# Kernel optimization log

Hardware: AMD Instinct MI355X
Metric: run time of the kernel (lower is better)

## Reference

```python
import jax, jax.numpy as jnp
import numpy as np
from functools import partial

EPS = 1e-6

def rmsnorm(x, w):
    rms = jnp.sqrt(jnp.mean(x * x, axis=-1, keepdims=True) + EPS)
    return x * w / rms

def causal_dwconv(x, w):
    # x: [B, T, D], w: [D, 1, k] depthwise kernel (torch Conv1d layout)
    D = x.shape[-1]
    k = w.shape[-1]
    xt = jnp.transpose(x, (0, 2, 1))  # [B, D, T]
    out = jax.lax.conv_general_dilated(
        xt, w, window_strides=(1,), padding=[(k - 1, 0)],
        dimension_numbers=("NCH", "OIH", "NCH"), feature_group_count=D)
    return jnp.transpose(out, (0, 2, 1))  # [B, T, D]

def setup_inputs() -> dict:
    key = jax.random.key(0)
    B, T, D, F, S = 2, 4096, 1024, 4096, 4096
    ks = jax.random.split(key, 20)
    s = 0.02
    return {
        "x": jax.random.normal(ks[0], (B, T, D), jnp.float32),
        "h_prev": jnp.zeros((B, D), jnp.float32),
        "norm1_w": jnp.ones((D,), jnp.float32),
        "conv3_w": jax.random.normal(ks[1], (D, 1, 3), jnp.float32) * s,
        "conv7_w": jax.random.normal(ks[2], (D, 1, 7), jnp.float32) * s,
        "conv15_w": jax.random.normal(ks[3], (D, 1, 15), jnp.float32) * s,
        "mix_w": jax.random.normal(ks[4], (D, D), jnp.float32) * s,
        "norm2_w": jnp.ones((D,), jnp.float32),
        "Wz_w": jax.random.normal(ks[5], (D, D), jnp.float32) * s,
        "Wz_b": jnp.zeros((D,), jnp.float32),
        "Wh_w": jax.random.normal(ks[6], (D, D), jnp.float32) * s,
        "Wh_b": jnp.zeros((D,), jnp.float32),
        "norm3_w": jnp.ones((D,), jnp.float32),
        "slot_keys": jax.random.normal(ks[7], (S, D), jnp.float32) * s,
        "slot_values": jax.random.normal(ks[8], (S, D), jnp.float32) * s,
        "projq_w": jax.random.normal(ks[9], (D, D), jnp.float32) * s,
        "projout_w": jax.random.normal(ks[10], (D, D), jnp.float32) * s,
        "norm4_w": jnp.ones((D,), jnp.float32),
        "gate_w": jax.random.normal(ks[11], (F, D), jnp.float32) * s,
        "up_w": jax.random.normal(ks[12], (F, D), jnp.float32) * s,
        "down_w": jax.random.normal(ks[13], (D, F), jnp.float32) * s,
    }

def resonance_forward(x, h_prev, norm1_w, conv3_w, conv7_w, conv15_w, mix_w,
                      norm2_w, Wz_w, Wz_b, Wh_w, Wh_b, norm3_w, slot_keys,
                      slot_values, projq_w, projout_w, norm4_w, gate_w, up_w, down_w):
    B, T, D = x.shape
    top_k = 2
    # 1. multi-scale causal conv block
    xn = rmsnorm(x, norm1_w)
    conv = causal_dwconv(xn, conv3_w) + causal_dwconv(xn, conv7_w) + causal_dwconv(xn, conv15_w)
    x = x + conv @ mix_w.T
    # 2. MinGRU: precompute gates, then linear recurrence via scan
    xn = rmsnorm(x, norm2_w)
    z = jax.nn.sigmoid(xn @ Wz_w.T + Wz_b)        # [B, T, D]
    h_tilde = xn @ Wh_w.T + Wh_b                  # [B, T, D]
    def step(h, zh):
        zt, ht = zh
        h = (1.0 - zt) * h + zt * ht
        return h, h
    h_last, hs = jax.lax.scan(step, h_prev,
                              (jnp.swapaxes(z, 0, 1), jnp.swapaxes(h_tilde, 0, 1)))
    x = x + jnp.swapaxes(hs, 0, 1)
    # 3. slot memory with top-k routing
    xn = rmsnorm(x, norm3_w)
    q = xn @ projq_w.T
    scores = (q @ slot_keys.T) / jnp.sqrt(jnp.asarray(D, x.dtype))  # [B, T, S]
    topk_vals, topk_ids = jax.lax.top_k(scores, top_k)              # [B, T, k]
    attn = jax.nn.softmax(topk_vals, axis=-1)
    gathered = slot_values[topk_ids]                                # [B, T, k, D]
    retrieved = jnp.einsum("btk,btkd->btd", attn, gathered)
    x = x + retrieved @ projout_w.T
    # 4. SwiGLU FFN
    xn = rmsnorm(x, norm4_w)
    ff = (jax.nn.silu(xn @ gate_w.T) * (xn @ up_w.T)) @ down_w.T
    x = x + ff
    return x, h_last

def reference(x, h_prev, norm1_w, conv3_w, conv7_w, conv15_w, mix_w, norm2_w,
              Wz_w, Wz_b, Wh_w, Wh_b, norm3_w, slot_keys, slot_values,
              projq_w, projout_w, norm4_w, gate_w, up_w, down_w):
    return resonance_forward(x, h_prev, norm1_w, conv3_w, conv7_w, conv15_w,
                             mix_w, norm2_w, Wz_w, Wz_b, Wh_w, Wh_b, norm3_w,
                             slot_keys, slot_values, projq_w, projout_w,
                             norm4_w, gate_w, up_w, down_w)
```

## Files before the change

kernel.cpp:

```cpp
#include <hip/hip_runtime.h>
#include <hip/hip_bf16.h>
#include <cstdint>
#include <cfloat>
#include <climits>

#define BB   2
#define TT   4096
#define DD   1024
#define FF   4096
#define SS   4096
#define MTOK (BB * TT)
#define NCHUNK 32
#define TCHUNK 128

typedef __bf16 bf16x8 __attribute__((ext_vector_type(8)));
typedef float  f32x4  __attribute__((ext_vector_type(4)));
typedef __attribute__((address_space(3))) char lds_char;
typedef __attribute__((address_space(1))) char g_char;

#define TKMERGE(w0, j0, w1, j1)                                              \
  {                                                                          \
    if (w0 > v0 || (w0 == v0 && j0 < i0)) {                                  \
      float t0v = v0; int t0i = i0; v0 = w0; i0 = j0;                        \
      if (t0v > w1 || (t0v == w1 && t0i < j1)) { v1 = t0v; i1 = t0i; }       \
      else { v1 = w1; i1 = j1; }                                             \
    } else {                                                                 \
      if (w0 > v1 || (w0 == v1 && j0 < i1)) { v1 = w0; i1 = j0; }            \
    }                                                                        \
  }

struct CvtArgs {
  const float* src[9];
  __hip_bfloat16* dst[9];
  int off4[10];
  int mode[9];
};

__global__ __launch_bounds__(256) void cvt_all_kernel(CvtArgs a) {
  int g = blockIdx.x * 256 + threadIdx.x;
  if (g >= a.off4[9]) return;
  int s = 0;
  while (g >= a.off4[s + 1]) s++;
  int i = g - a.off4[s];
  float4 v = ((const float4*)a.src[s])[i];
  union { ushort4 u; __hip_bfloat16 h[4]; } p;
  p.h[0] = __float2bfloat16(v.x);
  p.h[1] = __float2bfloat16(v.y);
  p.h[2] = __float2bfloat16(v.z);
  p.h[3] = __float2bfloat16(v.w);
  int di = i;
  int m = a.mode[s];
  if (m) {
    int r = i >> 8, c = i & 255;
    int dr = ((r >> 4) << 5) + (r & 15) + ((m == 2) ? 16 : 0);
    di = (dr << 8) + c;
  }
  ((ushort4*)a.dst[s])[di] = p.u;
}

__global__ void wcomb_kernel(const float* __restrict__ w3, const float* __restrict__ w7,
                             const float* __restrict__ w15, float* __restrict__ wc) {
  int d = blockIdx.x * 256 + threadIdx.x;
  if (d >= DD) return;
  for (int j = 0; j < 16; j++) {
    float v = 0.f;
    if (j < 15) {
      v = w15[d * 15 + (14 - j)];
      if (j < 7) v += w7[d * 7 + (6 - j)];
      if (j < 3) v += w3[d * 3 + (2 - j)];
    }
    wc[d * 16 + j] = v;
  }
}

__global__ __launch_bounds__(256) void rms_kernel(const float* __restrict__ x,
                                                  const float* __restrict__ w,
                                                  __hip_bfloat16* __restrict__ ob) {
  const int row = blockIdx.x;
  const int tid = threadIdx.x;
  float4 v = ((const float4*)(x + (size_t)row * DD))[tid];
  float ss = v.x * v.x + v.y * v.y + v.z * v.z + v.w * v.w;
  for (int off = 32; off > 0; off >>= 1) ss += __shfl_down(ss, off, 64);
  __shared__ float wsum[4];
  if ((tid & 63) == 0) wsum[tid >> 6] = ss;
  __syncthreads();
  float tot = wsum[0] + wsum[1] + wsum[2] + wsum[3];
  float rinv = 1.0f / sqrtf(tot * (1.0f / DD) + 1e-6f);
  float4 wg = ((const float4*)w)[tid];
  union { ushort4 u; __hip_bfloat16 h[4]; } p;
  p.h[0] = __float2bfloat16(v.x * wg.x * rinv);
  p.h[1] = __float2bfloat16(v.y * wg.y * rinv);
  p.h[2] = __float2bfloat16(v.z * wg.z * rinv);
  p.h[3] = __float2bfloat16(v.w * wg.w * rinv);
  ((ushort4*)ob)[(size_t)row * 256 + tid] = p.u;
}

__global__ __launch_bounds__(256) void conv_kernel(const __hip_bfloat16* __restrict__ xn,
                                                   const float* __restrict__ wc,
                                                   __hip_bfloat16* __restrict__ outp) {
  __shared__ float xt[78][64];
  __shared__ float wt[64][15];
  const int b = blockIdx.z, t0 = blockIdx.x * 64, d0 = blockIdx.y * 64;
  const int tid = threadIdx.x;
  const int dl = tid & 63;
  for (int idx = tid; idx < 64 * 15; idx += 256) {
    int d = idx / 15, j = idx % 15;
    wt[d][j] = wc[(d0 + d) * 16 + j];
  }
  for (int r = tid >> 6; r < 78; r += 4) {
    int t = t0 - 14 + r;
    xt[r][dl] = (t >= 0) ? __bfloat162float(xn[((size_t)b * TT + t) * DD + d0 + dl]) : 0.f;
  }
  __syncthreads();
  for (int tl = tid >> 6; tl < 64; tl += 4) {
    float acc = 0.f;
#pragma unroll
    for (int j = 0; j < 15; j++) acc += wt[dl][j] * xt[tl + 14 - j][dl];
    outp[((size_t)b * TT + t0 + tl) * DD + d0 + dl] = __float2bfloat16(acc);
  }
}

template <int EPI, int KSPLIT = 1, int SWZ = 0>
__global__ __launch_bounds__(256, 2) void gemm_bt(
    const __hip_bfloat16* __restrict__ A, const __hip_bfloat16* __restrict__ Bm,
    const int M, const int N, const int K,
    float* __restrict__ outf, __hip_bfloat16* __restrict__ outb,
    const float* __restrict__ bias0, const float* __restrict__ bias1) {
  __shared__ __align__(16) __hip_bfloat16 As[128 * 32];
  __shared__ __align__(16) __hip_bfloat16 Bs[128 * 32];
  const int tid = threadIdx.x;
  const int lane = tid & 63;
  const int wave = tid >> 6;
  const int fm = lane & 15, fq = lane >> 4;

  const int nT = gridDim.x;
  const int lin = blockIdx.y * nT + blockIdx.x;
  int tileM, tileN;
  if constexpr (SWZ == 0) {
    const int xcd = lin & 7;
    const int idx_ = lin >> 3;
    const int mq = idx_ / nT;
    tileM = (xcd * (gridDim.y >> 3) + mq) * 128;
    tileN = (idx_ - mq * nT) * 128;
  } else {
    const int xcd = lin & 7;
    const int idx_ = lin >> 3;
    const int nS = nT >> 3;
    const int m = idx_ / nS;
    const int nl = idx_ - m * nS;
    tileM = m * 128;
    tileN = (xcd * nS + nl) * 128;
  }

  const int wm = (wave & 1) * 64, wn = (wave >> 1) * 64;

  f32x4 acc[4][4] = {};

  const int srow = tid >> 2;
  const int scol = (tid & 3) * 8;
  const __hip_bfloat16* gA = A + (size_t)(tileM + srow) * K + scol;
  const __hip_bfloat16* gB = Bm + (size_t)(tileN + srow) * K + scol;
  lds_char* ldsA = (lds_char*)(&As[0]);
  lds_char* ldsB = (lds_char*)(&Bs[0]);
  const int wbyte = wave * 1024;

  const int kPer = K / KSPLIT;
  const int kBeg = (KSPLIT > 1) ? blockIdx.z * kPer : 0;
  for (int k0 = kBeg; k0 < kBeg + kPer; k0 += 32) {
    __syncthreads();
    __builtin_amdgcn_global_load_lds((g_char*)(void*)(gA + k0),                  ldsA + wbyte,        16, 0, 0);
    __builtin_amdgcn_global_load_lds((g_char*)(void*)(gA + k0 + (size_t)64 * K), ldsA + wbyte + 4096, 16, 0, 0);
    __builtin_amdgcn_global_load_lds((g_char*)(void*)(gB + k0),                  ldsB + wbyte,        16, 0, 0);
    __builtin_amdgcn_global_load_lds((g_char*)(void*)(gB + k0 + (size_t)64 * K), ldsB + wbyte + 4096, 16, 0, 0);
    __syncthreads();
    bf16x8 af[4], bfr[4];
#pragma unroll
    for (int i = 0; i < 4; i++) {
      af[i]  = *(const bf16x8*)(As + (wm + i * 16 + fm) * 32 + fq * 8);
      bfr[i] = *(const bf16x8*)(Bs + (wn + i * 16 + fm) * 32 + fq * 8);
    }
#pragma unroll
    for (int i = 0; i < 4; i++)
#pragma unroll
      for (int j = 0; j < 4; j++)
        acc[i][j] = __builtin_amdgcn_mfma_f32_16x16x32_bf16(af[i], bfr[j], acc[i][j], 0, 0, 0);
  }

  if constexpr (EPI == 7) {
#pragma unroll
    for (int i = 0; i < 4; i++) {
#pragma unroll
      for (int j = 0; j < 4; j += 2) {
        const int ffcol = (((tileN + wn + j * 16) >> 5) << 4) + fm;
#pragma unroll
        for (int r = 0; r < 4; r++) {
          const int rw = tileM + wm + i * 16 + fq * 4 + r;
          float g = acc[i][j][r];
          float u = acc[i][j + 1][r];
          float v = g / (1.f + __expf(-g)) * u;
          outb[(size_t)rw * FF + ffcol] = __float2bfloat16(v);
        }
      }
    }
  } else if constexpr (EPI == 8) {
    __syncthreads();
    __shared__ float lv[128][2];
    __shared__ int   li[128][2];
#pragma unroll
    for (int i = 0; i < 4; i++) {
#pragma unroll
      for (int r = 0; r < 4; r++) {
        float v0 = -FLT_MAX, v1 = -FLT_MAX;
        int i0 = INT_MAX, i1 = INT_MAX;
#pragma unroll
        for (int j = 0; j < 4; j++) {
          float v = acc[i][j][r];
          int c = tileN + wn + j * 16 + fm;
          if (v > v0) { v1 = v0; i1 = i0; v0 = v; i0 = c; }
          else if (v > v1) { v1 = v; i1 = c; }
        }
#pragma unroll
        for (int off = 1; off < 16; off <<= 1) {
          float w0 = __shfl_xor(v0, off, 64), w1 = __shfl_xor(v1, off, 64);
          int   j0 = __shfl_xor(i0, off, 64), j1 = __shfl_xor(i1, off, 64);
          TKMERGE(w0, j0, w1, j1);
        }
        const int lrow = wm + i * 16 + fq * 4 + r;
        if (wn == 64 && fm == 0) {
          lv[lrow][0] = v0; lv[lrow][1] = v1;
          li[lrow][0] = i0; li[lrow][1] = i1;
        }
      }
    }
    __syncthreads();
    if (wn == 0) {
#pragma unroll
      for (int i = 0; i < 4; i++) {
#pragma unroll
        for (int r = 0; r < 4; r++) {
          float v0 = -FLT_MAX, v1 = -FLT_MAX;
          int i0 = INT_MAX, i1 = INT_MAX;
#pragma unroll
          for (int j = 0; j < 4; j++) {
            float v = acc[i][j][r];
            int c = tileN + wn + j * 16 + fm;
            if (v > v0) { v1 = v0; i1 = i0; v0 = v; i0 = c; }
            else if (v > v1) { v1 = v; i1 = c; }
          }
#pragma unroll
          for (int off = 1; off < 16; off <<= 1) {
            float w0 = __shfl_xor(v0, off, 64), w1 = __shfl_xor(v1, off, 64);
            int   j0 = __shfl_xor(i0, off, 64), j1 = __shfl_xor(i1, off, 64);
            TKMERGE(w0, j0, w1, j1);
          }
          const int lrow = wm + i * 16 + fq * 4 + r;
          if (fm == 0) {
            float w0 = lv[lrow][0], w1 = lv[lrow][1];
            int   j0 = li[lrow][0], j1 = li[lrow][1];
            TKMERGE(w0, j0, w1, j1);
            float4 c4;
            c4.x = v0; c4.y = v1;
            c4.z = __int_as_float(i0); c4.w = __int_as_float(i1);
            ((float4*)outf)[(size_t)(tileM + lrow) * (SS / 128) + (tileN >> 7)] = c4;
          }
        }
      }
    }
  } else {
#pragma unroll
    for (int i = 0; i < 4; i++) {
#pragma unroll
      for (int j = 0; j < 4; j++) {
        const int c = tileN + wn + j * 16 + fm;
#pragma unroll
        for (int r = 0; r < 4; r++) {
          const int rw = tileM + wm + i * 16 + fq * 4 + r;
          const size_t idx = (size_t)rw * N + c;
          float v = acc[i][j][r];
          if constexpr (EPI == 1) {
            v += (c < DD) ? bias0[c] : bias1[c - DD];
            if (c < DD) v = 1.f / (1.f + __expf(-v));
            outb[idx] = __float2bfloat16(v);
          } else if constexpr (EPI == 2) {
            outb[idx] = __float2bfloat16(v);
          } else if constexpr (EPI == 6) {
            outf[(size_t)blockIdx.z * M * N + idx] = v;
          }
        }
      }
    }
  }
}

template <int EPI>
__global__ __launch_bounds__(256, 4) void gemm_bt64(
    const __hip_bfloat16* __restrict__ A, const __hip_bfloat16* __restrict__ Bm,
    const int M, const int N, const int K,
    const float* __restrict__ resid, float* __restrict__ outf,
    __hip_bfloat16* __restrict__ outb) {
  __shared__ __align__(16) __hip_bfloat16 As[64 * 32];
  __shared__ __align__(16) __hip_bfloat16 Bs[128 * 32];
  const int tid = threadIdx.x;
  const int lane = tid & 63;
  const int wave = tid >> 6;
  const int fm = lane & 15, fq = lane >> 4;

  const int nT = gridDim.x;
  const int lin = blockIdx.y * nT + blockIdx.x;
  const int xcd = lin & 7;
  const int idx_ = lin >> 3;
  const int mq = idx_ / nT;
  const int tileM = (xcd * (gridDim.y >> 3) + mq) * 64;
  const int tileN = (idx_ - mq * nT) * 128;

  const int wm = (wave & 1) * 32, wn = (wave >> 1) * 64;

  f32x4 acc[2][4] = {};

  const int srow = tid >> 2;
  const int scol = (tid & 3) * 8;
  const __hip_bfloat16* gA = A + (size_t)(tileM + srow) * K + scol;
  const __hip_bfloat16* gB = Bm + (size_t)(tileN + srow) * K + scol;
  lds_char* ldsA = (lds_char*)(&As[0]);
  lds_char* ldsB = (lds_char*)(&Bs[0]);
  const int wbyte = wave * 1024;

  for (int k0 = 0; k0 < K; k0 += 32) {
    __syncthreads();
    __builtin_amdgcn_global_load_lds((g_char*)(void*)(gA + k0),                  ldsA + wbyte,        16, 0, 0);
    __builtin_amdgcn_global_load_lds((g_char*)(void*)(gB + k0),                  ldsB + wbyte,        16, 0, 0);
    __builtin_amdgcn_global_load_lds((g_char*)(void*)(gB + k0 + (size_t)64 * K), ldsB + wbyte + 4096, 16, 0, 0);
    __syncthreads();
    bf16x8 af[2], bfr[4];
#pragma unroll
    for (int i = 0; i < 2; i++)
      af[i]  = *(const bf16x8*)(As + (wm + i * 16 + fm) * 32 + fq * 8);
#pragma unroll
    for (int j = 0; j < 4; j++)
      bfr[j] = *(const bf16x8*)(Bs + (wn + j * 16 + fm) * 32 + fq * 8);
#pragma unroll
    for (int i = 0; i < 2; i++)
#pragma unroll
      for (int j = 0; j < 4; j++)
        acc[i][j] = __builtin_amdgcn_mfma_f32_16x16x32_bf16(af[i], bfr[j], acc[i][j], 0, 0, 0);
  }

#pragma unroll
  for (int i = 0; i < 2; i++) {
#pragma unroll
    for (int j = 0; j < 4; j++) {
      const int c = tileN + wn + j * 16 + fm;
#pragma unroll
      for (int r = 0; r < 4; r++) {
        const int rw = tileM + wm + i * 16 + fq * 4 + r;
        const size_t idx = (size_t)rw * N + c;
        float v = acc[i][j][r];
        if constexpr (EPI == 0) {
          outf[idx] = resid[idx] + v;
        } else {
          outb[idx] = __float2bfloat16(v);
        }
      }
    }
  }
}

__global__ __launch_bounds__(256) void reduce_down(const float* __restrict__ P,
                                                   const float* __restrict__ resid,
                                                   float* __restrict__ out) {
  size_t i = (size_t)blockIdx.x * 256 + threadIdx.x;
  float4 a = ((const float4*)P)[i];
  float4 b = ((const float4*)(P + (size_t)MTOK * DD))[i];
  float4 rr = ((const float4*)resid)[i];
  float4 o;
  o.x = rr.x + a.x + b.x; o.y = rr.y + a.y + b.y;
  o.z = rr.z + a.z + b.z; o.w = rr.w + a.w + b.w;
  ((float4*)out)[i] = o;
}

__global__ __launch_bounds__(256) void scan_pass1(const __hip_bfloat16* __restrict__ zht,
                                                  float* __restrict__ cA,
                                                  float* __restrict__ cB) {
  const int b = blockIdx.z, c = blockIdx.y;
  const int d = blockIdx.x * 256 + threadIdx.x;
  const __hip_bfloat16* base = zht + (size_t)b * TT * 2048;
  float A = 1.f, Bc = 0.f;
  const int t0 = c * TCHUNK;
  for (int t = t0; t < t0 + TCHUNK; t++) {
    const __hip_bfloat16* rowp = base + (size_t)t * 2048;
    float z = __bfloat162float(rowp[d]);
    float h = __bfloat162float(rowp[DD + d]);
    float om = 1.f - z;
    A *= om;
    Bc = om * Bc + z * h;
  }
  size_t idx = ((size_t)b * NCHUNK + c) * DD + d;
  cA[idx] = A;
  cB[idx] = Bc;
}

__global__ __launch_bounds__(256) void scan_pass2(const float* __restrict__ hp,
                                                  const float* __restrict__ cA,
                                                  const float* __restrict__ cB,
                                                  float* __restrict__ hstart,
                                                  float* __restrict__ hlast) {
  const int b = blockIdx.y;
  const int d = blockIdx.x * 256 + threadIdx.x;
  float h = hp[b * DD + d];
  for (int c = 0; c < NCHUNK; c++) {
    size_t idx = ((size_t)b * NCHUNK + c) * DD + d;
    hstart[idx] = h;
    h = cA[idx] * h + cB[idx];
  }
  hlast[b * DD + d] = h;
}

__global__ __launch_bounds__(256) void scan_pass3(const __hip_bfloat16* __restrict__ zht,
                                                  const float* __restrict__ hstart,
                                                  float* __restrict__ x) {
  const int b = blockIdx.z, c = blockIdx.y;
  const int d = blockIdx.x * 256 + threadIdx.x;
  const __hip_bfloat16* base = zht + (size_t)b * TT * 2048;
  float h = hstart[((size_t)b * NCHUNK + c) * DD + d];
  const int t0 = c * TCHUNK;
  for (int t = t0; t < t0 + TCHUNK; t++) {
    const __hip_bfloat16* rowp = base + (size_t)t * 2048;
    float z = __bfloat162float(rowp[d]);
    float ht = __bfloat162float(rowp[DD + d]);
    h = (1.f - z) * h + z * ht;
    x[((size_t)b * TT + t) * DD + d] += h;
  }
}

__global__ __launch_bounds__(256) void topk_merge(const float4* __restrict__ cand,
                                                  const float* __restrict__ sv,
                                                  __hip_bfloat16* __restrict__ ret) {
  const int row = blockIdx.x * 4 + (threadIdx.x >> 6);
  const int lane = threadIdx.x & 63;
  float v0 = -FLT_MAX, v1 = -FLT_MAX;
  int i0 = INT_MAX, i1 = INT_MAX;
  if (lane < 32) {
    float4 c = cand[(size_t)row * 32 + lane];
    v0 = c.x; v1 = c.y;
    i0 = __float_as_int(c.z); i1 = __float_as_int(c.w);
  }
#pragma unroll
  for (int off = 1; off < 64; off <<= 1) {
    float w0 = __shfl_xor(v0, off, 64), w1 = __shfl_xor(v1, off, 64);
    int   j0 = __shfl_xor(i0, off, 64), j1 = __shfl_xor(i1, off, 64);
    TKMERGE(w0, j0, w1, j1);
  }
  float s0 = v0 * (1.f / 32.f), s1 = v1 * (1.f / 32.f);
  float e = __expf(s1 - s0);
  float denom = 1.f + e;
  float a0 = 1.f / denom;
  float a1 = e / denom;
  const float4* r0 = (const float4*)(sv + (size_t)i0 * DD);
  const float4* r1 = (const float4*)(sv + (size_t)i1 * DD);
#pragma unroll
  for (int k = 0; k < 4; k++) {
    int j = lane + 64 * k;
    float4 u = r0[j], w4 = r1[j];
    union { ushort4 u; __hip_bfloat16 h[4]; } p;
    p.h[0] = __float2bfloat16(a0 * u.x + a1 * w4.x);
    p.h[1] = __float2bfloat16(a0 * u.y + a1 * w4.y);
    p.h[2] = __float2bfloat16(a0 * u.z + a1 * w4.z);
    p.h[3] = __float2bfloat16(a0 * u.w + a1 * w4.w);
    ((ushort4*)(ret + (size_t)row * DD))[j] = p.u;
  }
}

extern "C" void kernel_launch(void* const* d_in, const int* in_sizes, int n_in,
                              void* d_out, int out_size, void* d_ws, size_t ws_size,
                              hipStream_t stream) {
  (void)in_sizes; (void)n_in; (void)out_size; (void)ws_size;
  const float* x_in   = (const float*)d_in[0];
  const float* h_prev = (const float*)d_in[1];
  const float* n1w    = (const float*)d_in[2];
  const float* w3     = (const float*)d_in[3];
  const float* w7     = (const float*)d_in[4];
  const float* w15    = (const float*)d_in[5];
  const float* mixw   = (const float*)d_in[6];
  const float* n2w    = (const float*)d_in[7];
  const float* wzw    = (const float*)d_in[8];
  const float* wzb    = (const float*)d_in[9];
  const float* whw    = (const float*)d_in[10];
  const float* whb    = (const float*)d_in[11];
  const float* n3w    = (const float*)d_in[12];
  const float* slotk  = (const float*)d_in[13];
  const float* slotv  = (const float*)d_in[14];
  const float* pqw    = (const float*)d_in[15];
  const float* pow_   = (const float*)d_in[16];
  const float* n4w    = (const float*)d_in[17];
  const float* gatew  = (const float*)d_in[18];
  const float* upw    = (const float*)d_in[19];
  const float* downw  = (const float*)d_in[20];
  float* out = (float*)d_out;

  char* ws = (char*)d_ws;
  size_t o = 0;
  auto alloc = [&](size_t bytes) {
    size_t r = o;
    o += (bytes + 255) & ~(size_t)255;
    return r;
  };
  __hip_bfloat16* wmix = (__hip_bfloat16*)(ws + alloc((size_t)DD * DD * 2));
  __hip_bfloat16* wzht = (__hip_bfloat16*)(ws + alloc((size_t)2 * DD * DD * 2));
  __hip_bfloat16* wpq  = (__hip_bfloat16*)(ws + alloc((size_t)DD * DD * 2));
  __hip_bfloat16* wsk  = (__hip_bfloat16*)(ws + alloc((size_t)SS * DD * 2));
  __hip_bfloat16* wpo  = (__hip_bfloat16*)(ws + alloc((size_t)DD * DD * 2));
  __hip_bfloat16* wfu  = (__hip_bfloat16*)(ws + alloc((size_t)2 * FF * DD * 2));
  __hip_bfloat16* wd   = (__hip_bfloat16*)(ws + alloc((size_t)DD * FF * 2));
  float* wcomb = (float*)(ws + alloc((size_t)DD * 16 * 4));
  float* xws   = (float*)(ws + alloc((size_t)MTOK * DD * 4));
  __hip_bfloat16* xnb  = (__hip_bfloat16*)(ws + alloc((size_t)MTOK * DD * 2));
  __hip_bfloat16* qb   = (__hip_bfloat16*)(ws + alloc((size_t)MTOK * DD * 2));
  __hip_bfloat16* retr = (__hip_bfloat16*)(ws + alloc((size_t)MTOK * DD * 2));
  float* scanA  = (float*)(ws + alloc((size_t)BB * NCHUNK * DD * 4));
  float* scanB  = (float*)(ws + alloc((size_t)BB * NCHUNK * DD * 4));
  float* hstart = (float*)(ws + alloc((size_t)BB * NCHUNK * DD * 4));
  char* big = ws + alloc((size_t)MTOK * FF * 4);
  __hip_bfloat16* xn1b  = (__hip_bfloat16*)big;
  __hip_bfloat16* convb = (__hip_bfloat16*)(big + (size_t)MTOK * DD * 2);
  __hip_bfloat16* zhtb  = (__hip_bfloat16*)big;
  float* candf          = (float*)big;
  __hip_bfloat16* ffin  = (__hip_bfloat16*)big;
  float* Pbuf           = (float*)(big + (size_t)MTOK * FF * 2);

  {
    CvtArgs a;
    const float* srcs[9] = {mixw, wzw, whw, pqw, slotk, pow_, gatew, upw, downw};
    __hip_bfloat16* dsts[9] = {wmix, wzht, wzht + (size_t)DD * DD, wpq, wsk, wpo, wfu, wfu, wd};
    int n4s[9] = {DD * DD / 4, DD * DD / 4, DD * DD / 4, DD * DD / 4, SS * DD / 4,
                  DD * DD / 4, FF * DD / 4, FF * DD / 4, DD * FF / 4};
    int modes[9] = {0, 0, 0, 0, 0, 0, 1, 2, 0};
    int acc_ = 0;
    for (int i = 0; i < 9; i++) {
      a.src[i] = srcs[i]; a.dst[i] = dsts[i]; a.off4[i] = acc_; a.mode[i] = modes[i];
      acc_ += n4s[i];
    }
    a.off4[9] = acc_;
    cvt_all_kernel<<<(acc_ + 255) / 256, 256, 0, stream>>>(a);
  }
  wcomb_kernel<<<DD / 256, 256, 0, stream>>>(w3, w7, w15, wcomb);

  rms_kernel<<<MTOK, 256, 0, stream>>>(x_in, n1w, xn1b);
  conv_kernel<<<dim3(TT / 64, DD / 64, BB), 256, 0, stream>>>(xn1b, wcomb, convb);
  gemm_bt64<0><<<dim3(DD / 128, MTOK / 64), 256, 0, stream>>>(
      convb, wmix, MTOK, DD, DD, x_in, xws, nullptr);

  rms_kernel<<<MTOK, 256, 0, stream>>>(xws, n2w, xnb);
  gemm_bt<1, 1, 1><<<dim3(2048 / 128, MTOK / 128), 256, 0, stream>>>(
      xnb, wzht, MTOK, 2048, DD, nullptr, zhtb, wzb, whb);
  scan_pass1<<<dim3(DD / 256, NCHUNK, BB), 256, 0, stream>>>(zhtb, scanA, scanB);
  scan_pass2<<<dim3(DD / 256, BB), 256, 0, stream>>>(h_prev, scanA, scanB, hstart,
                                                     out + (size_t)MTOK * DD);
  scan_pass3<<<dim3(DD / 256, NCHUNK, BB), 256, 0, stream>>>(zhtb, hstart, xws);

  rms_kernel<<<MTOK, 256, 0, stream>>>(xws, n3w, xnb);
  gemm_bt64<2><<<dim3(DD / 128, MTOK / 64), 256, 0, stream>>>(
      xnb, wpq, MTOK, DD, DD, nullptr, nullptr, qb);
  gemm_bt<8, 1, 1><<<dim3(SS / 128, MTOK / 128), 256, 0, stream>>>(
      qb, wsk, MTOK, SS, DD, candf, nullptr, nullptr, nullptr);
  topk_merge<<<MTOK / 4, 256, 0, stream>>>((const float4*)candf, slotv, retr);
  gemm_bt64<0><<<dim3(DD / 128, MTOK / 64), 256, 0, stream>>>(
      retr, wpo, MTOK, DD, DD, xws, xws, nullptr);

  rms_kernel<<<MTOK, 256, 0, stream>>>(xws, n4w, xnb);
  gemm_bt<7, 1, 1><<<dim3(2 * FF / 128, MTOK / 128), 256, 0, stream>>>(
      xnb, wfu, MTOK, 2 * FF, DD, nullptr, ffin, nullptr, nullptr);
  gemm_bt<6, 2, 0><<<dim3(DD / 128, MTOK / 128, 2), 256, 0, stream>>>(
      ffin, wd, MTOK, DD, FF, Pbuf, nullptr, nullptr, nullptr);
  reduce_down<<<MTOK * DD / 1024, 256, 0, stream>>>(Pbuf, xws, out);
}
```

Measured before the change: 813.7 us.

## Fold query projection into slot keys and simplify top-k epilogue merge

Precomputes slot_keys @ projq_w as a combined SxD weight (via a transposed bf16 copy of projq_w and an extra weight-side GEMM), so the per-token q projection GEMM is removed and scores come directly from the normalized activations. The top-k epilogue now has both column halves write their partial top-2 to shared memory and 128 threads do a single merge, instead of one half recomputing its reduction. A template parameter of the z/h gate GEMM is also changed. Folding the weights changes the bf16 rounding path, so near-tied top-k selections may differ, and the strided transpose writes in the conversion kernel are uncoalesced.

```diff
diff --git a/kernel.cpp b/kernel.cpp
--- a/kernel.cpp
+++ b/kernel.cpp
@@ -48,9 +48,16 @@
   p.h[1] = __float2bfloat16(v.y);
   p.h[2] = __float2bfloat16(v.z);
   p.h[3] = __float2bfloat16(v.w);
+  int m = a.mode[s];
+  if (m == 3) {
+    int r = i >> 8, c4 = i & 255;
+#pragma unroll
+    for (int k = 0; k < 4; k++)
+      a.dst[s][(size_t)(c4 * 4 + k) * 1024 + r] = p.h[k];
+    return;
+  }
   int di = i;
-  int m = a.mode[s];
-  if (m) {
+  if (m == 1 || m == 2) {
     int r = i >> 8, c = i & 255;
     int dr = ((r >> 4) << 5) + (r & 15) + ((m == 2) ? 16 : 0);
     di = (dr << 8) + c;
@@ -203,9 +210,9 @@
       }
     }
   } else if constexpr (EPI == 8) {
-    __syncthreads();
-    __shared__ float lv[128][2];
-    __shared__ int   li[128][2];
+    __shared__ float lv2[2][128][2];
+    __shared__ int   li2[2][128][2];
+    const int half = wn >> 6;
 #pragma unroll
     for (int i = 0; i < 4; i++) {
 #pragma unroll
@@ -225,46 +232,24 @@
           int   j0 = __shfl_xor(i0, off, 64), j1 = __shfl_xor(i1, off, 64);
           TKMERGE(w0, j0, w1, j1);
         }
-        const int lrow = wm + i * 16 + fq * 4 + r;
-        if (wn == 64 && fm == 0) {
-          lv[lrow][0] = v0; lv[lrow][1] = v1;
-          li[lrow][0] = i0; li[lrow][1] = i1;
+        if (fm == 0) {
+          const int lrow = wm + i * 16 + fq * 4 + r;
+          lv2[half][lrow][0] = v0; lv2[half][lrow][1] = v1;
+          li2[half][lrow][0] = i0; li2[half][lrow][1] = i1;
         }
       }
     }
     __syncthreads();
-    if (wn == 0) {
-#pragma unroll
-      for (int i = 0; i < 4; i++) {
-#pragma unroll
-        for (int r = 0; r < 4; r++) {
-          float v0 = -FLT_MAX, v1 = -FLT_MAX;
-          int i0 = INT_MAX, i1 = INT_MAX;
-#pragma unroll
-          for (int j = 0; j < 4; j++) {
-            float v = acc[i][j][r];
-            int c = tileN + wn + j * 16 + fm;
-            if (v > v0) { v1 = v0; i1 = i0; v0 = v; i0 = c; }
-            else if (v > v1) { v1 = v; i1 = c; }
-          }
-#pragma unroll
-          for (int off = 1; off < 16; off <<= 1) {
-            float w0 = __shfl_xor(v0, off, 64), w1 = __shfl_xor(v1, off, 64);
-            int   j0 = __shfl_xor(i0, off, 64), j1 = __shfl_xor(i1, off, 64);
-            TKMERGE(w0, j0, w1, j1);
-          }
-          const int lrow = wm + i * 16 + fq * 4 + r;
-          if (fm == 0) {
-            float w0 = lv[lrow][0], w1 = lv[lrow][1];
-            int   j0 = li[lrow][0], j1 = li[lrow][1];
-            TKMERGE(w0, j0, w1, j1);
-            float4 c4;
-            c4.x = v0; c4.y = v1;
-            c4.z = __int_as_float(i0); c4.w = __int_as_float(i1);
-            ((float4*)outf)[(size_t)(tileM + lrow) * (SS / 128) + (tileN >> 7)] = c4;
-          }
-        }
-      }
+    if (tid < 128) {
+      float v0 = lv2[0][tid][0], v1 = lv2[0][tid][1];
+      int   i0 = li2[0][tid][0], i1 = li2[0][tid][1];
+      float w0 = lv2[1][tid][0], w1 = lv2[1][tid][1];
+      int   j0 = li2[1][tid][0], j1 = li2[1][tid][1];
+      TKMERGE(w0, j0, w1, j1);
+      float4 c4;
+      c4.x = v0; c4.y = v1;
+      c4.z = __int_as_float(i0); c4.w = __int_as_float(i1);
+      ((float4*)outf)[(size_t)(tileM + tid) * (SS / 128) + (tileN >> 7)] = c4;
     }
   } else {
 #pragma unroll
@@ -506,15 +491,15 @@
   };
   __hip_bfloat16* wmix = (__hip_bfloat16*)(ws + alloc((size_t)DD * DD * 2));
   __hip_bfloat16* wzht = (__hip_bfloat16*)(ws + alloc((size_t)2 * DD * DD * 2));
-  __hip_bfloat16* wpq  = (__hip_bfloat16*)(ws + alloc((size_t)DD * DD * 2));
+  __hip_bfloat16* wpqT = (__hip_bfloat16*)(ws + alloc((size_t)DD * DD * 2));
   __hip_bfloat16* wsk  = (__hip_bfloat16*)(ws + alloc((size_t)SS * DD * 2));
   __hip_bfloat16* wpo  = (__hip_bfloat16*)(ws + alloc((size_t)DD * DD * 2));
   __hip_bfloat16* wfu  = (__hip_bfloat16*)(ws + alloc((size_t)2 * FF * DD * 2));
   __hip_bfloat16* wd   = (__hip_bfloat16*)(ws + alloc((size_t)DD * FF * 2));
+  __hip_bfloat16* w2b  = (__hip_bfloat16*)(ws + alloc((size_t)SS * DD * 2));
   float* wcomb = (float*)(ws + alloc((size_t)DD * 16 * 4));
   float* xws   = (float*)(ws + alloc((size_t)MTOK * DD * 4));
   __hip_bfloat16* xnb  = (__hip_bfloat16*)(ws + alloc((size_t)MTOK * DD * 2));
-  __hip_bfloat16* qb   = (__hip_bfloat16*)(ws + alloc((size_t)MTOK * DD * 2));
   __hip_bfloat16* retr = (__hip_bfloat16*)(ws + alloc((size_t)MTOK * DD * 2));
   float* scanA  = (float*)(ws + alloc((size_t)BB * NCHUNK * DD * 4));
   float* scanB  = (float*)(ws + alloc((size_t)BB * NCHUNK * DD * 4));
@@ -530,10 +515,10 @@
   {
     CvtArgs a;
     const float* srcs[9] = {mixw, wzw, whw, pqw, slotk, pow_, gatew, upw, downw};
-    __hip_bfloat16* dsts[9] = {wmix, wzht, wzht + (size_t)DD * DD, wpq, wsk, wpo, wfu, wfu, wd};
+    __hip_bfloat16* dsts[9] = {wmix, wzht, wzht + (size_t)DD * DD, wpqT, wsk, wpo, wfu, wfu, wd};
     int n4s[9] = {DD * DD / 4, DD * DD / 4, DD * DD / 4, DD * DD / 4, SS * DD / 4,
                   DD * DD / 4, FF * DD / 4, FF * DD / 4, DD * FF / 4};
-    int modes[9] = {0, 0, 0, 0, 0, 0, 1, 2, 0};
+    int modes[9] = {0, 0, 0, 3, 0, 0, 1, 2, 0};
     int acc_ = 0;
     for (int i = 0; i < 9; i++) {
       a.src[i] = srcs[i]; a.dst[i] = dsts[i]; a.off4[i] = acc_; a.mode[i] = modes[i];
@@ -543,6 +528,8 @@
     cvt_all_kernel<<<(acc_ + 255) / 256, 256, 0, stream>>>(a);
   }
   wcomb_kernel<<<DD / 256, 256, 0, stream>>>(w3, w7, w15, wcomb);
+  gemm_bt<2, 1, 0><<<dim3(DD / 128, SS / 128), 256, 0, stream>>>(
+      wsk, wpqT, SS, DD, DD, nullptr, w2b, nullptr, nullptr);
 
   rms_kernel<<<MTOK, 256, 0, stream>>>(x_in, n1w, xn1b);
   conv_kernel<<<dim3(TT / 64, DD / 64, BB), 256, 0, stream>>>(xn1b, wcomb, convb);
@@ -550,7 +537,7 @@
       convb, wmix, MTOK, DD, DD, x_in, xws, nullptr);
 
   rms_kernel<<<MTOK, 256, 0, stream>>>(xws, n2w, xnb);
-  gemm_bt<1, 1, 1><<<dim3(2048 / 128, MTOK / 128), 256, 0, stream>>>(
+  gemm_bt<1, 1, 0><<<dim3(2048 / 128, MTOK / 128), 256, 0, stream>>>(
       xnb, wzht, MTOK, 2048, DD, nullptr, zhtb, wzb, whb);
   scan_pass1<<<dim3(DD / 256, NCHUNK, BB), 256, 0, stream>>>(zhtb, scanA, scanB);
   scan_pass2<<<dim3(DD / 256, BB), 256, 0, stream>>>(h_prev, scanA, scanB, hstart,
@@ -558,10 +545,8 @@
   scan_pass3<<<dim3(DD / 256, NCHUNK, BB), 256, 0, stream>>>(zhtb, hstart, xws);
 
   rms_kernel<<<MTOK, 256, 0, stream>>>(xws, n3w, xnb);
-  gemm_bt64<2><<<dim3(DD / 128, MTOK / 64), 256, 0, stream>>>(
-      xnb, wpq, MTOK, DD, DD, nullptr, nullptr, qb);
   gemm_bt<8, 1, 1><<<dim3(SS / 128, MTOK / 128), 256, 0, stream>>>(
-      qb, wsk, MTOK, SS, DD, candf, nullptr, nullptr, nullptr);
+      xnb, w2b, MTOK, SS, DD, candf, nullptr, nullptr, nullptr);
   topk_merge<<<MTOK / 4, 256, 0, stream>>>((const float4*)candf, slotv, retr);
   gemm_bt64<0><<<dim3(DD / 128, MTOK / 64), 256, 0, stream>>>(
       retr, wpo, MTOK, DD, DD, xws, xws, nullptr);
```

After: 795.4 us. 1.02x faster.
